# Kernel optimization log

Hardware: AMD Instinct MI355X
Metric: run time of the kernel (lower is better)

Reference implementation:

```python
import jax, jax.numpy as jnp
import numpy as np

# sizes
N, B, NPG = 8192, 8, 1024          # total nodes, graphs, nodes per graph (equal-size graphs)
D, H, DH, L = 256, 8, 32, 2        # hidden, heads, head dim, layers
IN_C, OUT_D, E, DFF = 128, 64, 262144, 512
EPS = 1e-5


def setup_inputs() -> dict:
    key = jax.random.key(0)
    ks = jax.random.split(key, 20)
    p = lambda i, shp: jax.random.normal(ks[i], shp, jnp.float32) * 0.05
    return dict(
        x=jax.random.normal(ks[0], (N, IN_C), jnp.float32),
        edge_index=jax.random.randint(ks[1], (2, E), 0, N),
        batch=jnp.arange(N, dtype=jnp.int32) // NPG,  # sorted, equal-size graphs
        w_in=p(2, (D, IN_C)), b_in=p(3, (D,)),
        sage_wl=p(4, (L, D, D)), sage_bl=p(5, (L, D)), sage_wr=p(6, (L, D, D)),
        attn_iw=p(7, (L, 3 * D, D)), attn_ib=p(8, (L, 3 * D)),
        attn_ow=p(9, (L, D, D)), attn_ob=p(10, (L, D)),
        n1_w=jnp.ones((L, D)), n1_b=jnp.zeros((L, D)),
        n2_w=jnp.ones((L, D)), n2_b=jnp.zeros((L, D)),
        n3_w=jnp.ones((L, D)), n3_b=jnp.zeros((L, D)),
        mlp_w1=p(11, (L, DFF, D)), mlp_b1=p(12, (L, DFF)),
        mlp_w2=p(13, (L, D, DFF)), mlp_b2=p(14, (L, D)),
        bn_w=jnp.ones((L, D)), bn_b=jnp.zeros((L, D)),
        w_out=p(15, (OUT_D, D)), b_out=p(16, (OUT_D,)),
    )


def _bn(h, w, b):
    # BatchNorm1d over nodes (training-mode batch statistics, biased var)
    m = h.mean(0)
    v = jnp.mean((h - m) ** 2, axis=0)
    return (h - m) * jax.lax.rsqrt(v + EPS) * w + b


def _forward(x, edge_index, batch, w_in, b_in, sage_wl, sage_bl, sage_wr,
             attn_iw, attn_ib, attn_ow, attn_ob, n1_w, n1_b, n2_w, n2_b,
             n3_w, n3_b, mlp_w1, mlp_b1, mlp_w2, mlp_b2, bn_w, bn_b, w_out, b_out):
    src, dst = edge_index[0], edge_index[1]
    deg = jax.ops.segment_sum(jnp.ones((E,), jnp.float32), dst, num_segments=N)
    inv_deg = (1.0 / jnp.clip(deg, 1.0))[:, None]
    scale = 1.0 / np.sqrt(DH)

    h = x @ w_in.T + b_in  # in_proj Linear  [N, D]
    for l in range(L):
        # --- GPSConv: local SAGEConv (mean aggr) + residual + norm1 ---
        agg = jax.ops.segment_sum(h[src], dst, num_segments=N) * inv_deg
        loc = agg @ sage_wl[l].T + sage_bl[l] + h @ sage_wr[l].T
        loc = _bn(loc + h, n1_w[l], n1_b[l])
        # --- GPSConv: dense per-graph multi-head self-attention + residual + norm2 ---
        hd = h.reshape(B, NPG, D)  # to_dense_batch (no padding: equal graph sizes)
        qkv = hd @ attn_iw[l].T + attn_ib[l]  # [B, n, 3D]
        q, k, v = jnp.split(qkv, 3, axis=-1)
        sh = lambda t: t.reshape(B, NPG, H, DH).transpose(0, 2, 1, 3)  # [B, H, n, DH]
        a = jax.nn.softmax(jnp.einsum('bhqd,bhkd->bhqk', sh(q) * scale, sh(k)), axis=-1)
        o = jnp.einsum('bhqk,bhkd->bhqd', a, sh(v)).transpose(0, 2, 1, 3).reshape(B, NPG, D)
        o = (o @ attn_ow[l].T + attn_ob[l]).reshape(N, D)
        glob = _bn(o + h, n2_w[l], n2_b[l])
        # --- GPSConv: sum branches, MLP residual, norm3 ---
        out = loc + glob
        out = out + jax.nn.relu(out @ mlp_w1[l].T + mlp_b1[l]) @ mlp_w2[l].T + mlp_b2[l]
        out = _bn(out, n3_w[l], n3_b[l])
        # --- outer GPS: BatchNorm + relu + (dropout=eval) + residual ---
        h = h + jax.nn.relu(_bn(out, bn_w[l], bn_b[l]))
    pooled = h.reshape(B, NPG, D).mean(axis=1)  # global_mean_pool over sorted equal-size graphs
    return pooled @ w_out.T + b_out  # [B, OUT_D]


def reference(x, edge_index, batch, w_in, b_in, sage_wl, sage_bl, sage_wr,
              attn_iw, attn_ib, attn_ow, attn_ob, n1_w, n1_b, n2_w, n2_b,
              n3_w, n3_b, mlp_w1, mlp_b1, mlp_w2, mlp_b2, bn_w, bn_b, w_out, b_out):
    return _forward(x, edge_index, batch, w_in, b_in, sage_wl, sage_bl, sage_wr,
                    attn_iw, attn_ib, attn_ow, attn_ob, n1_w, n1_b, n2_w, n2_b,
                    n3_w, n3_b, mlp_w1, mlp_b1, mlp_w2, mlp_b2, bn_w, bn_b, w_out, b_out)
```

## Files before the change

### kernel.cpp

```cpp
#include <hip/hip_runtime.h>
#include <hip/hip_bf16.h>

#define N_NODES 8192
#define BGRAPH 8
#define NPG 1024
#define DIM 256
#define NH 8
#define DHEAD 32
#define NLAYERS 2
#define INC 128
#define OUTD 64
#define NEDGE 262144
#define DFF 512
#define EPS 1e-5f

typedef __attribute__((ext_vector_type(4))) float f32x4;
typedef __attribute__((ext_vector_type(8))) short s16x8;
typedef __attribute__((ext_vector_type(4))) ushort u16x4;

__device__ __forceinline__ float b2f(ushort u){
  unsigned v = ((unsigned)u) << 16;
  return __builtin_bit_cast(float, v);
}
__device__ __forceinline__ ushort f2b(float f){
  unsigned u = __builtin_bit_cast(unsigned, f);
  u += 0x7fffu + ((u >> 16) & 1u);
  return (ushort)(u >> 16);
}
__device__ __forceinline__ ushort f2b_trunc(float f){
  return (ushort)(__builtin_bit_cast(unsigned, f) >> 16);
}
__device__ __forceinline__ void gload16(const void* g, void* l){
  __builtin_amdgcn_global_load_lds(
    (const __attribute__((address_space(1))) void*)g,
    (__attribute__((address_space(3))) void*)l,
    16, 0, 0);
}

__global__ void k_count_deg(const int* __restrict__ dst, int* __restrict__ deg){
  int i = blockIdx.x*blockDim.x + threadIdx.x;
  int stride = gridDim.x*blockDim.x;
  for(; i<NEDGE; i+=stride) atomicAdd(&deg[dst[i]], 1);
}
__global__ void k_scan(const int* __restrict__ deg, int* __restrict__ offs,
                       float* __restrict__ inv_deg){
  __shared__ int s[1024];
  int t = threadIdx.x;
  int base = t*8;
  int loc[8]; int acc=0;
  #pragma unroll
  for(int j=0;j<8;j++){
    int dv = deg[base+j];
    inv_deg[base+j] = 1.0f/(float)(dv>0?dv:1);
    loc[j]=acc; acc += dv;
  }
  s[t]=acc;
  __syncthreads();
  for(int d=1; d<1024; d<<=1){
    int v = (t>=d)? s[t-d] : 0;
    __syncthreads();
    if(t>=d) s[t]+=v;
    __syncthreads();
  }
  int pre = (t>0)? s[t-1] : 0;
  #pragma unroll
  for(int j=0;j<8;j++) offs[base+j] = pre + loc[j];
  if(t==1023) offs[N_NODES] = s[1023];
}
__global__ void k_fill_csr(const int* __restrict__ src, const int* __restrict__ dst,
                           const int* __restrict__ offs, int* __restrict__ cursor,
                           int* __restrict__ csr){
  int i = blockIdx.x*blockDim.x + threadIdx.x;
  int stride = gridDim.x*blockDim.x;
  for(; i<NEDGE; i+=stride){
    int d = dst[i];
    int p = atomicAdd(&cursor[d], 1);
    csr[offs[d]+p] = src[i];
  }
}

__global__ __launch_bounds__(256) void k_aggregate(ushort* __restrict__ hwb,
    const int* __restrict__ offs, const int* __restrict__ csr,
    const float* __restrict__ inv_deg){
  int n = blockIdx.x*4 + (threadIdx.x>>6);
  int lane = threadIdx.x & 63;
  int beg = offs[n], end = offs[n+1];
  f32x4 a0 = {0,0,0,0}, a1 = {0,0,0,0}, a2 = {0,0,0,0}, a3 = {0,0,0,0};
  int i = beg;
  for(; i+4<=end; i+=4){
    int j0=csr[i], j1=csr[i+1], j2=csr[i+2], j3=csr[i+3];
    u16x4 v0 = *(const u16x4*)(hwb + (size_t)j0*512 + 256 + lane*4);
    u16x4 v1 = *(const u16x4*)(hwb + (size_t)j1*512 + 256 + lane*4);
    u16x4 v2 = *(const u16x4*)(hwb + (size_t)j2*512 + 256 + lane*4);
    u16x4 v3 = *(const u16x4*)(hwb + (size_t)j3*512 + 256 + lane*4);
    #pragma unroll
    for(int c=0;c<4;c++){ a0[c]+=b2f(v0[c]); a1[c]+=b2f(v1[c]);
                          a2[c]+=b2f(v2[c]); a3[c]+=b2f(v3[c]); }
  }
  for(; i<end; ++i){
    int j0=csr[i];
    u16x4 v0 = *(const u16x4*)(hwb + (size_t)j0*512 + 256 + lane*4);
    #pragma unroll
    for(int c=0;c<4;c++) a0[c]+=b2f(v0[c]);
  }
  float inv = inv_deg[n];
  u16x4 outv;
  #pragma unroll
  for(int c=0;c<4;c++) outv[c] = f2b((a0[c]+a1[c]+a2[c]+a3[c])*inv);
  *(u16x4*)(hwb + (size_t)n*512 + lane*4) = outv;
}

#define STAGE_AB(t, buf) do{ \
    int kt_ = (t)*64; \
    _Pragma("unroll") \
    for(int it=0; it<2; ++it){ \
      int c = (wave*2+it)*64 + lane; \
      int row = c >> 3, q = c & 7; \
      int qs = q ^ (row & 7); \
      gload16(A + (size_t)(bm+row)*lda + kt_ + qs*8, (char*)As + (buf)*8192 + (wave*2+it)*1024); \
      gload16(W + (size_t)(bn+row)*K   + kt_ + qs*8, (char*)Bs + (buf)*8192 + (wave*2+it)*1024); \
    } \
  }while(0)

template<bool RELU, bool RESID, bool RESIDB, bool BIAS, bool WF32, bool WBF, bool STATS>
__global__ __launch_bounds__(256) void k_mm(const ushort* __restrict__ A,
    const ushort* __restrict__ W, const float* __restrict__ bias,
    const float* __restrict__ resid, const ushort* __restrict__ residb,
    float* __restrict__ Cf, ushort* __restrict__ Cb,
    float* __restrict__ gS, float* __restrict__ gQ,
    int M, int Nc, int K, int lda, int ldcb)
{
  __shared__ ushort As[3*64*64];
  __shared__ ushort Bs[3*64*64];
  __shared__ float sredS[64];
  __shared__ float sredQ[64];
  const int tid = threadIdx.x;
  const int lane = tid & 63, wave = tid >> 6;
  const int l15 = lane & 15, l4 = lane >> 4;
  const int bm = blockIdx.y*64, bn = blockIdx.x*64;
  const int wr = wave >> 1, wc = wave & 1;
  f32x4 acc[2][2] = {};
  const int nt = K >> 6;

  STAGE_AB(0, 0);
  if(nt > 1) STAGE_AB(1, 1);

  for(int t=0; t<nt; ++t){
    int cb = t % 3;
    if(t+2 < nt){
      STAGE_AB(t+2, (t+2)%3);
      asm volatile("s_waitcnt vmcnt(8)" ::: "memory");
    } else if(t+1 < nt){
      asm volatile("s_waitcnt vmcnt(4)" ::: "memory");
    } else {
      asm volatile("s_waitcnt vmcnt(0)" ::: "memory");
    }
    __builtin_amdgcn_s_barrier();
    #pragma unroll
    for(int kk=0; kk<2; ++kk){
      s16x8 af[2], bfr[2];
      #pragma unroll
      for(int mi=0; mi<2; ++mi){
        int row = wr*32 + mi*16 + l15;
        int col = (kk*64 + l4*16) ^ ((row & 7) << 4);
        af[mi] = *(const s16x8*)((const char*)As + cb*8192 + row*128 + col);
      }
      #pragma unroll
      for(int nj=0; nj<2; ++nj){
        int row = wc*32 + nj*16 + l15;
        int col = (kk*64 + l4*16) ^ ((row & 7) << 4);
        bfr[nj] = *(const s16x8*)((const char*)Bs + cb*8192 + row*128 + col);
      }
      #pragma unroll
      for(int mi=0; mi<2; ++mi)
        #pragma unroll
        for(int nj=0; nj<2; ++nj)
          acc[mi][nj] = __builtin_amdgcn_mfma_f32_16x16x32_bf16(af[mi], bfr[nj], acc[mi][nj], 0,0,0);
    }
    asm volatile("s_waitcnt lgkmcnt(0)" ::: "memory");
    __builtin_amdgcn_s_barrier();
  }

  float sloc[2] = {0.f,0.f}, qloc[2] = {0.f,0.f};
  #pragma unroll
  for(int mi=0; mi<2; ++mi){
    #pragma unroll
    for(int nj=0; nj<2; ++nj){
      int col = bn + wc*32 + nj*16 + l15;
      float bv = BIAS ? bias[col] : 0.f;
      #pragma unroll
      for(int r=0; r<4; ++r){
        int row = bm + wr*32 + mi*16 + l4*4 + r;
        size_t off = (size_t)row*Nc + col;
        float v = acc[mi][nj][r] + bv;
        if(RESID)  v += resid[off];
        if(RESIDB) v += b2f(residb[off]);
        if(RELU)   v = fmaxf(v, 0.f);
        if(WF32)   Cf[off] = v;
        if(WBF)    Cb[(size_t)row*ldcb + col] = f2b(v);
        if(STATS){ sloc[nj] += v; qloc[nj] += v*v; }
      }
    }
  }
  if(STATS){
    if(tid < 64){ sredS[tid]=0.f; sredQ[tid]=0.f; }
    __syncthreads();
    int c0 = wc*32 + l15;
    atomicAdd(&sredS[c0],    sloc[0]); atomicAdd(&sredQ[c0],    qloc[0]);
    atomicAdd(&sredS[c0+16], sloc[1]); atomicAdd(&sredQ[c0+16], qloc[1]);
    __syncthreads();
    if(tid < 64){
      atomicAdd(&gS[bn+tid], sredS[tid]);
      atomicAdd(&gQ[bn+tid], sredQ[tid]);
    }
  }
}

__global__ __launch_bounds__(256) void k_attn(const ushort* __restrict__ qkv,
                                              ushort* __restrict__ attnO)
{
  __shared__ ushort Ks[2][64*32];
  __shared__ ushort Vt[2][32*64];
  const int tid = threadIdx.x, lane = tid & 63, wave = tid >> 6;
  const int l15 = lane & 15, g = lane >> 4;
  int bid = blockIdx.x;
  int qc = bid & 15;
  int h  = (bid >> 4) & 7;
  int bg = bid >> 7;
  const int nb = bg*NPG + qc*64 + wave*16;
  const int kb = bg*NPG;

  const int rho = tid >> 2, qq = tid & 3;
  const int grp = rho >> 5, r32 = rho & 31;
  const int tt = r32 >> 4, wi = r32 & 15;
  const int jperm = grp*32 + (wi >> 2)*8 + tt*4 + (wi & 3);
  const int qs = qq ^ ((rho >> 1) & 3);

  s16x8 qf = *(const s16x8*)(qkv + (size_t)(nb + l15)*768 + h*32 + g*8);
  {
    const float scale2 = 0.2550370703637335f;
    #pragma unroll
    for(int i=0;i<8;i++) qf[i] = (short)f2b(b2f((ushort)qf[i]) * scale2);
  }
  f32x4 o0 = {0.f,0.f,0.f,0.f}, o1 = {0.f,0.f,0.f,0.f};
  float mrun = -1e30f, lrun = 0.f;

  gload16(qkv + (size_t)(kb + jperm)*768 + 256 + h*32 + qs*8, (char*)Ks[0] + wave*1024);
  s16x8 vcur = *(const s16x8*)(qkv + (size_t)(kb + lane)*768 + 512 + h*32 + wave*8);

  for(int st=0; st<16; ++st){
    int buf = st & 1;
    #pragma unroll
    for(int i=0;i<8;i++){
      int d = wave*8 + i;
      Vt[buf][d*64 + (lane ^ (i<<3))] = (ushort)vcur[i];
    }
    s16x8 vnext = vcur;
    if(st+1 < 16){
      gload16(qkv + (size_t)(kb + (st+1)*64 + jperm)*768 + 256 + h*32 + qs*8,
              (char*)Ks[buf^1] + wave*1024);
      vnext = *(const s16x8*)(qkv + (size_t)(kb + (st+1)*64 + lane)*768 + 512 + h*32 + wave*8);
      asm volatile("s_waitcnt vmcnt(2) lgkmcnt(0)" ::: "memory");
    } else {
      asm volatile("s_waitcnt vmcnt(0) lgkmcnt(0)" ::: "memory");
    }
    __builtin_amdgcn_s_barrier();

    f32x4 sc[4];
    __builtin_amdgcn_s_setprio(1);
    #pragma unroll
    for(int q4=0; q4<4; ++q4){
      int r0 = q4*16 + l15;
      s16x8 kf = *(const s16x8*)((const char*)Ks[buf] + r0*64 + ((g*16) ^ (((r0>>1)&3)<<4)));
      f32x4 z = {0.f,0.f,0.f,0.f};
      sc[q4] = __builtin_amdgcn_mfma_f32_16x16x32_bf16(kf, qf, z, 0,0,0);
    }
    __builtin_amdgcn_s_setprio(0);

    float smax = -1e30f;
    #pragma unroll
    for(int q4=0; q4<4; ++q4)
      #pragma unroll
      for(int r=0; r<4; ++r) smax = fmaxf(smax, sc[q4][r]);
    smax = fmaxf(smax, __shfl_xor(smax, 16));
    smax = fmaxf(smax, __shfl_xor(smax, 32));

    if(!__all((int)(smax <= mrun + 8.0f))){
      float mnew = fmaxf(mrun, smax);
      float alpha = exp2f(mrun - mnew);
      lrun *= alpha;
      #pragma unroll
      for(int r=0;r<4;r++){
        float ar = __shfl(alpha, (lane & 48) | (g*4 + r), 64);
        o0[r] *= ar; o1[r] *= ar;
      }
      mrun = mnew;
    }

    float p[16];
    float ps = 0.f;
    #pragma unroll
    for(int q4=0; q4<4; ++q4)
      #pragma unroll
      for(int r=0; r<4; ++r){
        float pv = exp2f(sc[q4][r] - mrun);
        p[q4*4+r] = pv; ps += pv;
      }
    ps += __shfl_xor(ps, 16);
    ps += __shfl_xor(ps, 32);
    lrun += ps;

    s16x8 pa0, pa1;
    #pragma unroll
    for(int i=0;i<8;i++){ pa0[i] = (short)f2b_trunc(p[i]); pa1[i] = (short)f2b_trunc(p[8+i]); }

    int colb0 = g*16, colb1 = 64 + g*16;
    int d0 = l15, d1 = l15 + 16;
    s16x8 v00 = *(const s16x8*)((const char*)Vt[buf] + d0*128 + (colb0 ^ ((d0&7)<<4)));
    s16x8 v01 = *(const s16x8*)((const char*)Vt[buf] + d1*128 + (colb0 ^ ((d1&7)<<4)));
    s16x8 v10 = *(const s16x8*)((const char*)Vt[buf] + d0*128 + (colb1 ^ ((d0&7)<<4)));
    s16x8 v11 = *(const s16x8*)((const char*)Vt[buf] + d1*128 + (colb1 ^ ((d1&7)<<4)));
    __builtin_amdgcn_s_setprio(1);
    o0 = __builtin_amdgcn_mfma_f32_16x16x32_bf16(pa0, v00, o0, 0,0,0);
    o1 = __builtin_amdgcn_mfma_f32_16x16x32_bf16(pa0, v01, o1, 0,0,0);
    o0 = __builtin_amdgcn_mfma_f32_16x16x32_bf16(pa1, v10, o0, 0,0,0);
    o1 = __builtin_amdgcn_mfma_f32_16x16x32_bf16(pa1, v11, o1, 0,0,0);
    __builtin_amdgcn_s_setprio(0);

    asm volatile("s_waitcnt lgkmcnt(0)" ::: "memory");
    __builtin_amdgcn_s_barrier();
    vcur = vnext;
  }
  float inv = 1.0f/lrun;
  #pragma unroll
  for(int r=0;r<4;r++){
    int q2 = g*4 + r;
    float ir = __shfl(inv, (lane & 48) | q2, 64);
    size_t nrow = (size_t)(nb + q2)*DIM + h*32;
    attnO[nrow + l15]      = f2b(o0[r]*ir);
    attnO[nrow + 16 + l15] = f2b(o1[r]*ir);
  }
}

__global__ __launch_bounds__(256) void k_apply12(const float* __restrict__ locC,
    const float* __restrict__ globC, const float* __restrict__ slot,
    const float* __restrict__ n1w, const float* __restrict__ n1b,
    const float* __restrict__ n2w, const float* __restrict__ n2b,
    ushort* __restrict__ combB){
  int d = threadIdx.x;
  size_t i = (size_t)blockIdx.x*DIM + d;
  const float invn = 1.0f/N_NODES;
  float m1 = slot[d]*invn,     v1 = slot[256+d]*invn - m1*m1;
  float m2 = slot[512+d]*invn, v2 = slot[768+d]*invn - m2*m2;
  float rs1 = rsqrtf(v1+EPS), rs2 = rsqrtf(v2+EPS);
  float y1 = (locC[i]-m1)*rs1*n1w[d] + n1b[d];
  float y2 = (globC[i]-m2)*rs2*n2w[d] + n2b[d];
  combB[i] = f2b(y1 + y2);
}

__global__ __launch_bounds__(256) void k_apply3o(const float* __restrict__ x,
    const float* __restrict__ slot, const float* __restrict__ n3w,
    const float* __restrict__ n3b, const float* __restrict__ bw,
    const float* __restrict__ bb, float* __restrict__ H,
    ushort* __restrict__ hwbR){
  int d = threadIdx.x;
  size_t i = (size_t)blockIdx.x*DIM + d;
  const float invn = 1.0f/N_NODES;
  float m   = slot[1024+d]*invn;
  float var = slot[1280+d]*invn - m*m;
  float rs  = rsqrtf(var+EPS);
  float gch = rs*n3w[d];
  float rso = rsqrtf(gch*gch*var + EPS);
  float yo = (x[i]-m)*gch*rso*bw[d] + bb[d];
  float h = H[i] + fmaxf(yo, 0.f);
  H[i] = h;
  hwbR[(size_t)blockIdx.x*512 + d] = f2b(h);
}

#define CX  1048576
#define CWI (CX+32768)
#define CSW (CWI+262144)
#define CIW (CSW+393216)
#define COW (CIW+131072)
#define CW1 (COW+262144)
#define CW2 (CW1+262144)
__global__ void k_cast_all(const float* __restrict__ x, const float* __restrict__ w_in,
    const float* __restrict__ wl, const float* __restrict__ wr,
    const float* __restrict__ iw, const float* __restrict__ ow,
    const float* __restrict__ w1, const float* __restrict__ w2,
    ushort* __restrict__ dst){
  int i = blockIdx.x*256 + threadIdx.x;
  float val;
  if(i < CX)       val = x[i];
  else if(i < CWI) val = w_in[i-CX];
  else if(i < CSW){
    int j = i - CWI;
    int l = j >> 17, r = (j >> 9) & 255, k = j & 511;
    val = (k < 256) ? wl[(l<<16) + (r<<8) + k] : wr[(l<<16) + (r<<8) + (k-256)];
  }
  else if(i < CIW) val = iw[i-CSW];
  else if(i < COW) val = ow[i-CIW];
  else if(i < CW1) val = w1[i-COW];
  else             val = w2[i-CW1];
  dst[i] = f2b(val);
}

__global__ void k_pool(const float* __restrict__ h, float* __restrict__ pooled){
  int b = blockIdx.x, c = blockIdx.y, d = threadIdx.x;
  int r0 = c*64;
  float s=0.f;
  for(int i=0;i<64;i++) s += h[(size_t)(b*NPG + r0 + i)*DIM + d];
  atomicAdd(&pooled[b*DIM+d], s*(1.0f/NPG));
}
__global__ void k_out(const float* __restrict__ pooled, const float* __restrict__ w_out,
                      const float* __restrict__ b_out, float* __restrict__ out){
  int t = threadIdx.x;
  if(t >= BGRAPH*OUTD) return;
  int b = t/OUTD, oc = t%OUTD;
  float s = b_out[oc];
  for(int k=0;k<DIM;k++) s += pooled[b*DIM+k]*w_out[oc*DIM+k];
  out[t] = s;
}

extern "C" void kernel_launch(void* const* d_in, const int* in_sizes, int n_in,
                              void* d_out, int out_size, void* d_ws, size_t ws_size,
                              hipStream_t stream) {
  const float* x       = (const float*)d_in[0];
  const int*   edge    = (const int*)d_in[1];
  const float* w_in    = (const float*)d_in[3];
  const float* b_in    = (const float*)d_in[4];
  const float* sage_wl = (const float*)d_in[5];
  const float* sage_bl = (const float*)d_in[6];
  const float* sage_wr = (const float*)d_in[7];
  const float* attn_iw = (const float*)d_in[8];
  const float* attn_ib = (const float*)d_in[9];
  const float* attn_ow = (const float*)d_in[10];
  const float* attn_ob = (const float*)d_in[11];
  const float* n1_w = (const float*)d_in[12];
  const float* n1_b = (const float*)d_in[13];
  const float* n2_w = (const float*)d_in[14];
  const float* n2_b = (const float*)d_in[15];
  const float* n3_w = (const float*)d_in[16];
  const float* n3_b = (const float*)d_in[17];
  const float* mlp_w1 = (const float*)d_in[18];
  const float* mlp_b1 = (const float*)d_in[19];
  const float* mlp_w2 = (const float*)d_in[20];
  const float* mlp_b2 = (const float*)d_in[21];
  const float* bn_w = (const float*)d_in[22];
  const float* bn_b = (const float*)d_in[23];
  const float* w_out = (const float*)d_in[24];
  const float* b_out = (const float*)d_in[25];

  const size_t ND = (size_t)N_NODES*DIM;
  float* ws    = (float*)d_ws;
  float* H     = ws;
  float* locC  = ws + ND;
  float* globC = ws + 2*ND;
  ushort* wsb   = (ushort*)(ws + 3*ND);
  ushort* hwb   = wsb;
  ushort* qkvb  = wsb + 2*ND;
  ushort* attnOb= wsb + 5*ND;
  ushort* combb = wsb + 6*ND;
  ushort* hidb  = wsb + 7*ND;
  ushort* castb = wsb + 9*ND;
  ushort* xb     = castb;
  ushort* w_in_b = castb + CX;
  ushort* sageWb = castb + CWI;
  ushort* iw_b   = castb + CSW;
  ushort* ow_b   = castb + CIW;
  ushort* w1_b   = castb + COW;
  ushort* w2_b   = castb + CW1;
  float* mf      = (float*)(castb + CW2);
  float* inv_deg = mf;
  float* bnslots = mf + 8192;
  float* pooled  = bnslots + 3072;
  int* deg    = (int*)(pooled + 2048);
  int* cursor = deg + N_NODES;
  int* offs   = cursor + N_NODES;
  int* csr    = offs + N_NODES + 8;

  const int* esrc = edge;
  const int* edst = edge + NEDGE;

  hipMemsetAsync(bnslots, 0, (3072+2048)*sizeof(float) + 2*N_NODES*sizeof(int), stream);

  k_count_deg<<<512,256,0,stream>>>(edst, deg);
  k_scan<<<1,1024,0,stream>>>(deg, offs, inv_deg);
  k_fill_csr<<<512,256,0,stream>>>(esrc, edst, offs, cursor, csr);
  k_cast_all<<<CW2/256,256,0,stream>>>(x, w_in, sage_wl, sage_wr, attn_iw,
      attn_ow, mlp_w1, mlp_w2, castb);

  k_mm<false,false,false,true,true,true,false><<<dim3(4,128),256,0,stream>>>(
      xb, w_in_b, b_in, nullptr, nullptr, H, hwb+256, nullptr, nullptr,
      N_NODES, DIM, INC, INC, 512);

  for(int l=0; l<NLAYERS; ++l){
    const ushort* swb = sageWb + (size_t)l*131072;
    const ushort* iwb = iw_b + (size_t)l*196608;
    const ushort* owb = ow_b + (size_t)l*65536;
    const ushort* w1b = w1_b + (size_t)l*131072;
    const ushort* w2b = w2_b + (size_t)l*131072;
    float* slot = bnslots + (size_t)l*1536;

    k_aggregate<<<N_NODES/4,256,0,stream>>>(hwb, offs, csr, inv_deg);
    k_mm<false,true,false,true,true,false,true><<<dim3(4,128),256,0,stream>>>(
        hwb, swb, sage_bl + l*DIM, H, nullptr, locC, nullptr, slot, slot+256,
        N_NODES, DIM, 512, 512, 0);

    k_mm<false,false,false,true,false,true,false><<<dim3(12,128),256,0,stream>>>(
        hwb+256, iwb, attn_ib + l*3*DIM, nullptr, nullptr, nullptr, qkvb,
        nullptr, nullptr, N_NODES, 3*DIM, DIM, 512, 768);
    k_attn<<<1024,256,0,stream>>>(qkvb, attnOb);
    k_mm<false,true,false,true,true,false,true><<<dim3(4,128),256,0,stream>>>(
        attnOb, owb, attn_ob + l*DIM, H, nullptr, globC, nullptr, slot+512, slot+768,
        N_NODES, DIM, DIM, DIM, 0);

    k_apply12<<<N_NODES,256,0,stream>>>(locC, globC, slot,
        n1_w + l*DIM, n1_b + l*DIM, n2_w + l*DIM, n2_b + l*DIM, combb);

    k_mm<true,false,false,true,false,true,false><<<dim3(8,128),256,0,stream>>>(
        combb, w1b, mlp_b1 + l*DFF, nullptr, nullptr, nullptr, hidb,
        nullptr, nullptr, N_NODES, DFF, DIM, DIM, 512);
    k_mm<false,false,true,true,true,false,true><<<dim3(4,128),256,0,stream>>>(
        hidb, w2b, mlp_b2 + l*DIM, nullptr, combb, globC, nullptr,
        slot+1024, slot+1280, N_NODES, DIM, 512, 512, 0);

    k_apply3o<<<N_NODES,256,0,stream>>>(globC, slot, n3_w + l*DIM, n3_b + l*DIM,
        bn_w + l*DIM, bn_b + l*DIM, H, hwb+256);
  }

  k_pool<<<dim3(BGRAPH, NPG/64),256,0,stream>>>(H, pooled);
  k_out<<<1,512,0,stream>>>(pooled, w_out, b_out, (float*)d_out);
}
```

Measured before the change: 314.2 us.

## Store GEMM outputs in bf16, merge setup kernels, double-buffer GEMM, remap attention blocks

Several unrelated changes land together. The degree-count and weight-cast kernels become one launch, and pooling plus the output projection become one kernel. The fp32 intermediates locC/globC are now stored as bf16, which halves their write and read traffic at some cost in precision before the batch-norm applies. The GEMM drops from triple to double buffering with a full vmcnt wait at the end of each iteration, and the attention block index is remapped so heads and graphs vary fastest. The GEMM change may expose more load latency, and the single-block-per-graph pooling kernel runs with only eight blocks.

```diff
diff --git a/kernel.cpp b/kernel.cpp
--- a/kernel.cpp
+++ b/kernel.cpp
@@ -37,11 +37,41 @@
     16, 0, 0);
 }
 
-__global__ void k_count_deg(const int* __restrict__ dst, int* __restrict__ deg){
-  int i = blockIdx.x*blockDim.x + threadIdx.x;
-  int stride = gridDim.x*blockDim.x;
-  for(; i<NEDGE; i+=stride) atomicAdd(&deg[dst[i]], 1);
-}
+#define CX  1048576
+#define CWI (CX+32768)
+#define CSW (CWI+262144)
+#define CIW (CSW+393216)
+#define COW (CIW+131072)
+#define CW1 (COW+262144)
+#define CW2 (CW1+262144)
+#define NCAST (CW2/256)
+__global__ void k_setup(const float* __restrict__ x, const float* __restrict__ w_in,
+    const float* __restrict__ wl, const float* __restrict__ wr,
+    const float* __restrict__ iw, const float* __restrict__ ow,
+    const float* __restrict__ w1, const float* __restrict__ w2,
+    ushort* __restrict__ dst, const int* __restrict__ edst, int* __restrict__ deg){
+  if(blockIdx.x >= NCAST){
+    int i = (blockIdx.x - NCAST)*256 + threadIdx.x;
+    int stride = 512*256;
+    for(; i<NEDGE; i+=stride) atomicAdd(&deg[edst[i]], 1);
+    return;
+  }
+  int i = blockIdx.x*256 + threadIdx.x;
+  float val;
+  if(i < CX)       val = x[i];
+  else if(i < CWI) val = w_in[i-CX];
+  else if(i < CSW){
+    int j = i - CWI;
+    int l = j >> 17, r = (j >> 9) & 255, k = j & 511;
+    val = (k < 256) ? wl[(l<<16) + (r<<8) + k] : wr[(l<<16) + (r<<8) + (k-256)];
+  }
+  else if(i < CIW) val = iw[i-CSW];
+  else if(i < COW) val = ow[i-CIW];
+  else if(i < CW1) val = w1[i-COW];
+  else             val = w2[i-CW1];
+  dst[i] = f2b(val);
+}
+
 __global__ void k_scan(const int* __restrict__ deg, int* __restrict__ offs,
                        float* __restrict__ inv_deg){
   __shared__ int s[1024];
@@ -130,8 +160,8 @@
     float* __restrict__ gS, float* __restrict__ gQ,
     int M, int Nc, int K, int lda, int ldcb)
 {
-  __shared__ ushort As[3*64*64];
-  __shared__ ushort Bs[3*64*64];
+  __shared__ ushort As[2*64*64];
+  __shared__ ushort Bs[2*64*64];
   __shared__ float sredS[64];
   __shared__ float sredQ[64];
   const int tid = threadIdx.x;
@@ -143,19 +173,12 @@
   const int nt = K >> 6;
 
   STAGE_AB(0, 0);
-  if(nt > 1) STAGE_AB(1, 1);
-
+  asm volatile("s_waitcnt vmcnt(0)" ::: "memory");
+  __builtin_amdgcn_s_barrier();
+
+  int cur = 0;
   for(int t=0; t<nt; ++t){
-    int cb = t % 3;
-    if(t+2 < nt){
-      STAGE_AB(t+2, (t+2)%3);
-      asm volatile("s_waitcnt vmcnt(8)" ::: "memory");
-    } else if(t+1 < nt){
-      asm volatile("s_waitcnt vmcnt(4)" ::: "memory");
-    } else {
-      asm volatile("s_waitcnt vmcnt(0)" ::: "memory");
-    }
-    __builtin_amdgcn_s_barrier();
+    if(t+1 < nt) STAGE_AB(t+1, cur^1);
     #pragma unroll
     for(int kk=0; kk<2; ++kk){
       s16x8 af[2], bfr[2];
@@ -163,13 +186,13 @@
       for(int mi=0; mi<2; ++mi){
         int row = wr*32 + mi*16 + l15;
         int col = (kk*64 + l4*16) ^ ((row & 7) << 4);
-        af[mi] = *(const s16x8*)((const char*)As + cb*8192 + row*128 + col);
+        af[mi] = *(const s16x8*)((const char*)As + cur*8192 + row*128 + col);
       }
       #pragma unroll
       for(int nj=0; nj<2; ++nj){
         int row = wc*32 + nj*16 + l15;
         int col = (kk*64 + l4*16) ^ ((row & 7) << 4);
-        bfr[nj] = *(const s16x8*)((const char*)Bs + cb*8192 + row*128 + col);
+        bfr[nj] = *(const s16x8*)((const char*)Bs + cur*8192 + row*128 + col);
       }
       #pragma unroll
       for(int mi=0; mi<2; ++mi)
@@ -177,8 +200,9 @@
         for(int nj=0; nj<2; ++nj)
           acc[mi][nj] = __builtin_amdgcn_mfma_f32_16x16x32_bf16(af[mi], bfr[nj], acc[mi][nj], 0,0,0);
     }
-    asm volatile("s_waitcnt lgkmcnt(0)" ::: "memory");
+    asm volatile("s_waitcnt vmcnt(0)" ::: "memory");
     __builtin_amdgcn_s_barrier();
+    cur ^= 1;
   }
 
   float sloc[2] = {0.f,0.f}, qloc[2] = {0.f,0.f};
@@ -224,9 +248,9 @@
   const int tid = threadIdx.x, lane = tid & 63, wave = tid >> 6;
   const int l15 = lane & 15, g = lane >> 4;
   int bid = blockIdx.x;
-  int qc = bid & 15;
-  int h  = (bid >> 4) & 7;
-  int bg = bid >> 7;
+  int h  = bid & 7;
+  int bg = (bid >> 3) & 7;
+  int qc = bid >> 6;
   const int nb = bg*NPG + qc*64 + wave*16;
   const int kb = bg*NPG;
 
@@ -342,8 +366,8 @@
   }
 }
 
-__global__ __launch_bounds__(256) void k_apply12(const float* __restrict__ locC,
-    const float* __restrict__ globC, const float* __restrict__ slot,
+__global__ __launch_bounds__(256) void k_apply12(const ushort* __restrict__ locB,
+    const ushort* __restrict__ globB, const float* __restrict__ slot,
     const float* __restrict__ n1w, const float* __restrict__ n1b,
     const float* __restrict__ n2w, const float* __restrict__ n2b,
     ushort* __restrict__ combB){
@@ -353,12 +377,12 @@
   float m1 = slot[d]*invn,     v1 = slot[256+d]*invn - m1*m1;
   float m2 = slot[512+d]*invn, v2 = slot[768+d]*invn - m2*m2;
   float rs1 = rsqrtf(v1+EPS), rs2 = rsqrtf(v2+EPS);
-  float y1 = (locC[i]-m1)*rs1*n1w[d] + n1b[d];
-  float y2 = (globC[i]-m2)*rs2*n2w[d] + n2b[d];
+  float y1 = (b2f(locB[i])-m1)*rs1*n1w[d] + n1b[d];
+  float y2 = (b2f(globB[i])-m2)*rs2*n2w[d] + n2b[d];
   combB[i] = f2b(y1 + y2);
 }
 
-__global__ __launch_bounds__(256) void k_apply3o(const float* __restrict__ x,
+__global__ __launch_bounds__(256) void k_apply3o(const ushort* __restrict__ xB,
     const float* __restrict__ slot, const float* __restrict__ n3w,
     const float* __restrict__ n3b, const float* __restrict__ bw,
     const float* __restrict__ bb, float* __restrict__ H,
@@ -371,55 +395,28 @@
   float rs  = rsqrtf(var+EPS);
   float gch = rs*n3w[d];
   float rso = rsqrtf(gch*gch*var + EPS);
-  float yo = (x[i]-m)*gch*rso*bw[d] + bb[d];
+  float yo = (b2f(xB[i])-m)*gch*rso*bw[d] + bb[d];
   float h = H[i] + fmaxf(yo, 0.f);
   H[i] = h;
   hwbR[(size_t)blockIdx.x*512 + d] = f2b(h);
 }
 
-#define CX  1048576
-#define CWI (CX+32768)
-#define CSW (CWI+262144)
-#define CIW (CSW+393216)
-#define COW (CIW+131072)
-#define CW1 (COW+262144)
-#define CW2 (CW1+262144)
-__global__ void k_cast_all(const float* __restrict__ x, const float* __restrict__ w_in,
-    const float* __restrict__ wl, const float* __restrict__ wr,
-    const float* __restrict__ iw, const float* __restrict__ ow,
-    const float* __restrict__ w1, const float* __restrict__ w2,
-    ushort* __restrict__ dst){
-  int i = blockIdx.x*256 + threadIdx.x;
-  float val;
-  if(i < CX)       val = x[i];
-  else if(i < CWI) val = w_in[i-CX];
-  else if(i < CSW){
-    int j = i - CWI;
-    int l = j >> 17, r = (j >> 9) & 255, k = j & 511;
-    val = (k < 256) ? wl[(l<<16) + (r<<8) + k] : wr[(l<<16) + (r<<8) + (k-256)];
-  }
-  else if(i < CIW) val = iw[i-CSW];
-  else if(i < COW) val = ow[i-CIW];
-  else if(i < CW1) val = w1[i-COW];
-  else             val = w2[i-CW1];
-  dst[i] = f2b(val);
-}
-
-__global__ void k_pool(const float* __restrict__ h, float* __restrict__ pooled){
-  int b = blockIdx.x, c = blockIdx.y, d = threadIdx.x;
-  int r0 = c*64;
-  float s=0.f;
-  for(int i=0;i<64;i++) s += h[(size_t)(b*NPG + r0 + i)*DIM + d];
-  atomicAdd(&pooled[b*DIM+d], s*(1.0f/NPG));
-}
-__global__ void k_out(const float* __restrict__ pooled, const float* __restrict__ w_out,
-                      const float* __restrict__ b_out, float* __restrict__ out){
-  int t = threadIdx.x;
-  if(t >= BGRAPH*OUTD) return;
-  int b = t/OUTD, oc = t%OUTD;
-  float s = b_out[oc];
-  for(int k=0;k<DIM;k++) s += pooled[b*DIM+k]*w_out[oc*DIM+k];
-  out[t] = s;
+__global__ __launch_bounds__(256) void k_pool_out(const float* __restrict__ H,
+    const float* __restrict__ w_out, const float* __restrict__ b_out,
+    float* __restrict__ out){
+  __shared__ float pl[256];
+  int b = blockIdx.x, d = threadIdx.x;
+  float s = 0.f;
+  const float* base = H + (size_t)b*NPG*DIM + d;
+  for(int r=0; r<NPG; ++r) s += base[(size_t)r*DIM];
+  pl[d] = s * (1.0f/NPG);
+  __syncthreads();
+  if(d < OUTD){
+    float acc = b_out[d];
+    #pragma unroll 4
+    for(int k=0; k<DIM; ++k) acc += pl[k]*w_out[d*DIM+k];
+    out[b*OUTD + d] = acc;
+  }
 }
 
 extern "C" void kernel_launch(void* const* d_in, const int* in_sizes, int n_in,
@@ -454,15 +451,15 @@
   const size_t ND = (size_t)N_NODES*DIM;
   float* ws    = (float*)d_ws;
   float* H     = ws;
-  float* locC  = ws + ND;
-  float* globC = ws + 2*ND;
-  ushort* wsb   = (ushort*)(ws + 3*ND);
-  ushort* hwb   = wsb;
-  ushort* qkvb  = wsb + 2*ND;
-  ushort* attnOb= wsb + 5*ND;
-  ushort* combb = wsb + 6*ND;
-  ushort* hidb  = wsb + 7*ND;
-  ushort* castb = wsb + 9*ND;
+  ushort* wsb   = (ushort*)(ws + ND);
+  ushort* locB  = wsb;
+  ushort* globB = wsb + ND;
+  ushort* hwb   = wsb + 2*ND;
+  ushort* qkvb  = wsb + 4*ND;
+  ushort* attnOb= wsb + 7*ND;
+  ushort* combb = wsb + 8*ND;
+  ushort* hidb  = wsb + 9*ND;
+  ushort* castb = wsb + 11*ND;
   ushort* xb     = castb;
   ushort* w_in_b = castb + CX;
   ushort* sageWb = castb + CWI;
@@ -473,8 +470,7 @@
   float* mf      = (float*)(castb + CW2);
   float* inv_deg = mf;
   float* bnslots = mf + 8192;
-  float* pooled  = bnslots + 3072;
-  int* deg    = (int*)(pooled + 2048);
+  int* deg    = (int*)(bnslots + 3072);
   int* cursor = deg + N_NODES;
   int* offs   = cursor + N_NODES;
   int* csr    = offs + N_NODES + 8;
@@ -482,13 +478,12 @@
   const int* esrc = edge;
   const int* edst = edge + NEDGE;
 
-  hipMemsetAsync(bnslots, 0, (3072+2048)*sizeof(float) + 2*N_NODES*sizeof(int), stream);
-
-  k_count_deg<<<512,256,0,stream>>>(edst, deg);
+  hipMemsetAsync(bnslots, 0, 3072*sizeof(float) + 2*N_NODES*sizeof(int), stream);
+
+  k_setup<<<NCAST+512,256,0,stream>>>(x, w_in, sage_wl, sage_wr, attn_iw,
+      attn_ow, mlp_w1, mlp_w2, castb, edst, deg);
   k_scan<<<1,1024,0,stream>>>(deg, offs, inv_deg);
   k_fill_csr<<<512,256,0,stream>>>(esrc, edst, offs, cursor, csr);
-  k_cast_all<<<CW2/256,256,0,stream>>>(x, w_in, sage_wl, sage_wr, attn_iw,
-      attn_ow, mlp_w1, mlp_w2, castb);
 
   k_mm<false,false,false,true,true,true,false><<<dim3(4,128),256,0,stream>>>(
       xb, w_in_b, b_in, nullptr, nullptr, H, hwb+256, nullptr, nullptr,
@@ -503,32 +498,31 @@
     float* slot = bnslots + (size_t)l*1536;
 
     k_aggregate<<<N_NODES/4,256,0,stream>>>(hwb, offs, csr, inv_deg);
-    k_mm<false,true,false,true,true,false,true><<<dim3(4,128),256,0,stream>>>(
-        hwb, swb, sage_bl + l*DIM, H, nullptr, locC, nullptr, slot, slot+256,
-        N_NODES, DIM, 512, 512, 0);
+    k_mm<false,true,false,true,false,true,true><<<dim3(4,128),256,0,stream>>>(
+        hwb, swb, sage_bl + l*DIM, H, nullptr, nullptr, locB, slot, slot+256,
+        N_NODES, DIM, 512, 512, DIM);
 
     k_mm<false,false,false,true,false,true,false><<<dim3(12,128),256,0,stream>>>(
         hwb+256, iwb, attn_ib + l*3*DIM, nullptr, nullptr, nullptr, qkvb,
         nullptr, nullptr, N_NODES, 3*DIM, DIM, 512, 768);
     k_attn<<<1024,256,0,stream>>>(qkvb, attnOb);
-    k_mm<false,true,false,true,true,false,true><<<dim3(4,128),256,0,stream>>>(
-        attnOb, owb, attn_ob + l*DIM, H, nullptr, globC, nullptr, slot+512, slot+768,
-        N_NODES, DIM, DIM, DIM, 0);
-
-    k_apply12<<<N_NODES,256,0,stream>>>(locC, globC, slot,
+    k_mm<false,true,false,true,false,true,true><<<dim3(4,128),256,0,stream>>>(
+        attnOb, owb, attn_ob + l*DIM, H, nullptr, nullptr, globB, slot+512, slot+768,
+        N_NODES, DIM, DIM, DIM, DIM);
+
+    k_apply12<<<N_NODES,256,0,stream>>>(locB, globB, slot,
         n1_w + l*DIM, n1_b + l*DIM, n2_w + l*DIM, n2_b + l*DIM, combb);
 
     k_mm<true,false,false,true,false,true,false><<<dim3(8,128),256,0,stream>>>(
         combb, w1b, mlp_b1 + l*DFF, nullptr, nullptr, nullptr, hidb,
         nullptr, nullptr, N_NODES, DFF, DIM, DIM, 512);
-    k_mm<false,false,true,true,true,false,true><<<dim3(4,128),256,0,stream>>>(
-        hidb, w2b, mlp_b2 + l*DIM, nullptr, combb, globC, nullptr,
-        slot+1024, slot+1280, N_NODES, DIM, 512, 512, 0);
-
-    k_apply3o<<<N_NODES,256,0,stream>>>(globC, slot, n3_w + l*DIM, n3_b + l*DIM,
+    k_mm<false,false,true,true,false,true,true><<<dim3(4,128),256,0,stream>>>(
+        hidb, w2b, mlp_b2 + l*DIM, nullptr, combb, nullptr, globB,
+        slot+1024, slot+1280, N_NODES, DIM, 512, 512, DIM);
+
+    k_apply3o<<<N_NODES,256,0,stream>>>(globB, slot, n3_w + l*DIM, n3_b + l*DIM,
         bn_w + l*DIM, bn_b + l*DIM, H, hwb+256);
   }
 
-  k_pool<<<dim3(BGRAPH, NPG/64),256,0,stream>>>(H, pooled);
-  k_out<<<1,512,0,stream>>>(pooled, w_out, b_out, (float*)d_out);
-}
+  k_pool_out<<<BGRAPH,256,0,stream>>>(H, w_out, b_out, (float*)d_out);
+}
```

Result: no change. 320.4 us (+1.9%).
